# Optimization experiments

Measured on AMD Instinct MI355X. Metric: run time of the kernel, lower is better.

## Reference

```python
import jax, jax.numpy as jnp
import numpy as np

NA, NQ, FDIM, NC, HID = 512, 4096, 2, 16, 64
CUTOFF = 6.0
GAMMA = 10.0
BOX = 12.0


def setup_inputs() -> dict:
    key = jax.random.key(0)
    ks = jax.random.split(key, 16)
    s = lambda k, shp, fan: jax.random.normal(k, shp, jnp.float32) * (1.0 / np.sqrt(fan))
    return {
        "atom_pos": jax.random.uniform(ks[0], (NA, 3), jnp.float32) * BOX,
        "atom_feat": jax.random.normal(ks[1], (NA, FDIM), jnp.float32),
        "query_pos": jax.random.uniform(ks[2], (NQ, 3), jnp.float32) * BOX,
        "W1": s(ks[3], (FDIM + NC, HID), FDIM + NC), "b1": jnp.zeros((HID,), jnp.float32),
        "W2": s(ks[4], (HID, HID), HID), "b2": jnp.zeros((HID,), jnp.float32),
        "W3": s(ks[5], (HID, HID // 2), HID), "b3": jnp.zeros((HID // 2,), jnp.float32),
        "W4": s(ks[6], (HID // 2, 1), HID // 2), "b4": jnp.zeros((1,), jnp.float32),
        "W5": s(ks[7], (3, 64), 3), "b5": jnp.zeros((64,), jnp.float32),
        "W6": s(ks[8], (64, 3), 64), "b6": jnp.zeros((3,), jnp.float32),
    }


def _forward(atom_pos, atom_feat, query_pos, W1, b1, W2, b2, W3, b3, W4, b4, W5, b5, W6, b6):
    centers = jnp.linspace(0.0, CUTOFF, NC, dtype=jnp.float32)  # RBF centers
    rel = query_pos[:, None, :] - atom_pos[None, :, :]          # (Nq,Na,3)
    dist = jnp.linalg.norm(rel + 1e-12, axis=-1)                 # (Nq,Na) (matches torch.norm(rel+eps))
    mask = (dist <= CUTOFF).astype(dist.dtype)
    rbf = jnp.exp(-GAMMA * (dist[..., None] - centers) ** 2)     # (Nq,Na,Nc)
    feat_b = jnp.broadcast_to(atom_feat[None], (query_pos.shape[0],) + atom_feat.shape)
    atom_input = jnp.concatenate([feat_b, rbf], axis=-1)         # (Nq,Na,F+Nc)
    h = jax.nn.relu(atom_input @ W1 + b1)
    h = jax.nn.relu(h @ W2 + b2)                                 # (Nq,Na,H)
    scalar_w = (jax.nn.relu(h @ W3 + b3) @ W4 + b4)[..., 0] * mask  # (Nq,Na)
    dir_vec = rel / (dist[..., None] + 1e-12)                    # (Nq,Na,3)
    weighted = jnp.einsum('qa,qad->qd', scalar_w, dir_vec)       # (Nq,3)
    out = jax.nn.relu(weighted @ W5 + b5) @ W6 + b6              # (Nq,3)
    return out


def reference(atom_pos, atom_feat, query_pos, W1, b1, W2, b2, W3, b3, W4, b4, W5, b5, W6, b6):
    return _forward(atom_pos, atom_feat, query_pos, W1, b1, W2, b2, W3, b3, W4, b4, W5, b5, W6, b6)
```

## Files before the change

### kernel.cpp

```cpp
#include <hip/hip_runtime.h>
#include <math.h>


typedef _Float16 f16x4 __attribute__((ext_vector_type(4)));
typedef _Float16 f16x2 __attribute__((ext_vector_type(2)));
typedef float    f32x4 __attribute__((ext_vector_type(4)));

#define CAP 352
#define NT  2

__global__ __launch_bounds__(64) void repack_kernel(
    const float* __restrict__ W1, const float* __restrict__ b1,
    const float* __restrict__ W2, const float* __restrict__ b2,
    const float* __restrict__ W3, const float* __restrict__ b3,
    const float* __restrict__ W4, char* __restrict__ ws)
{
    const int b = blockIdx.x, l = threadIdx.x;
    const int col = l & 15, quad = l >> 4;
    if (b < 32) {
        f16x4 v;
        #pragma unroll
        for (int j = 0; j < 4; ++j) {
            float x;
            if (b < 8) {
                const int kc = b >> 2, mt = b & 3;
                const int k = kc*16 + quad*4 + j;
                x = (k < 18) ? W1[k*64 + mt*16 + col]
                             : (k == 18 ? b1[mt*16 + col] : 0.0f);
            } else if (b < 24) {
                const int idx = b - 8, kc = idx >> 2, mt = idx & 3;
                const int k = kc*16 + quad*4 + j;
                x = W2[k*64 + mt*16 + col];
            } else {
                const int idx = b - 24, kc = idx >> 1, mt = idx & 1;
                const int k = kc*16 + quad*4 + j;
                x = W3[k*32 + mt*16 + col];
            }
            v[j] = (_Float16)x;
        }
        *(f16x4*)(ws + (b*64 + l)*8) = v;
    } else {
        const int d = b - 32;
        float o[4];
        #pragma unroll
        for (int rr = 0; rr < 4; ++rr) {
            const int idx = quad*4 + rr;
            if (d < 4)      o[rr] = b2[d*16 + idx];
            else if (d < 6) o[rr] = b3[(d-4)*16 + idx];
            else            o[rr] = W4[(d-6)*16 + idx];
        }
        *(float4*)(ws + 16384 + (d*64 + l)*16) = make_float4(o[0],o[1],o[2],o[3]);
    }
}

__device__ __forceinline__ f16x4 relu_cvt(f32x4 c) {
    return f16x4{(_Float16)fmaxf(c[0],0.f), (_Float16)fmaxf(c[1],0.f),
                 (_Float16)fmaxf(c[2],0.f), (_Float16)fmaxf(c[3],0.f)};
}

__global__ __launch_bounds__(256, 1) void aqfn_kernel(
    const float* __restrict__ atom_pos,
    const float* __restrict__ atom_feat,
    const float* __restrict__ query_pos,
    const float* __restrict__ b4,
    const float* __restrict__ W5, const float* __restrict__ b5,
    const float* __restrict__ W6, const float* __restrict__ b6,
    const char*  __restrict__ ws,
    float* __restrict__ out)
{
    __shared__ __align__(16) float4 rbuf[CAP];
    __shared__ __align__(16) f16x2  fbuf[CAP];
    __shared__ float wred[4][3];
    __shared__ int   wcnt[4];

    const int tid  = threadIdx.x;
    const int wave = __builtin_amdgcn_readfirstlane(tid >> 6);
    const int lane = tid & 63;
    const int col  = lane & 15;
    const int quad = lane >> 4;
    const int q    = blockIdx.x;

    const f16x4*  wsf = (const f16x4*)ws;
    const float4* wsb = (const float4*)(ws + 16384);
    f16x4 w1f[2][4], w2f[4][4], w3f[4][2];
    #pragma unroll
    for (int kc = 0; kc < 2; ++kc)
        #pragma unroll
        for (int mt = 0; mt < 4; ++mt) w1f[kc][mt] = wsf[(kc*4 + mt)*64 + lane];
    #pragma unroll
    for (int kc = 0; kc < 4; ++kc)
        #pragma unroll
        for (int mt = 0; mt < 4; ++mt) w2f[kc][mt] = wsf[(8 + kc*4 + mt)*64 + lane];
    #pragma unroll
    for (int kc = 0; kc < 4; ++kc)
        #pragma unroll
        for (int mt = 0; mt < 2; ++mt) w3f[kc][mt] = wsf[(24 + kc*2 + mt)*64 + lane];
    float4 b2v[4], b3v[2], w4v[2];
    #pragma unroll
    for (int mt = 0; mt < 4; ++mt) b2v[mt] = wsb[mt*64 + lane];
    #pragma unroll
    for (int mt = 0; mt < 2; ++mt) { b3v[mt] = wsb[(4+mt)*64 + lane];
                                     w4v[mt] = wsb[(6+mt)*64 + lane]; }
    const float b4v = b4[0];

    const float qx = query_pos[q*3+0];
    const float qy = query_pos[q*3+1];
    const float qz = query_pos[q*3+2];

    float rxv[2], ryv[2], rzv[2], dv[2], f0v[2], f1v[2];
    unsigned long long msk[2];
    int mycnt = 0;
    #pragma unroll
    for (int it = 0; it < 2; ++it) {
        const int a = wave*128 + it*64 + lane;
        const float rx = qx - atom_pos[a*3+0];
        const float ry = qy - atom_pos[a*3+1];
        const float rz = qz - atom_pos[a*3+2];
        const float ex = __fadd_rn(rx, 1e-12f);
        const float ey = __fadd_rn(ry, 1e-12f);
        const float ez = __fadd_rn(rz, 1e-12f);
        const float dd = __fadd_rn(__fadd_rn(__fmul_rn(ex,ex), __fmul_rn(ey,ey)),
                                   __fmul_rn(ez,ez));
        const float dist = sqrtf(dd);
        rxv[it] = rx; ryv[it] = ry; rzv[it] = rz; dv[it] = dist;
        f0v[it] = atom_feat[a*2+0]; f1v[it] = atom_feat[a*2+1];
        msk[it] = __ballot(dist <= 6.0f);
        mycnt  += (int)__popcll(msk[it]);
    }
    if (lane == 0) wcnt[wave] = mycnt;
    __syncthreads();

    int base = 0, count = 0;
    #pragma unroll
    for (int w = 0; w < 4; ++w) {
        const int c = wcnt[w];
        if (w < wave) base += c;
        count += c;
    }
    if (count > CAP) count = CAP;

    {
        int off0 = base;
        #pragma unroll
        for (int it = 0; it < 2; ++it) {
            const bool in = (msk[it] >> lane) & 1ull;
            const int  p  = off0 + (int)__popcll(msk[it] & ((1ull << lane) - 1ull));
            if (in && p < CAP) {
                rbuf[p] = make_float4(rxv[it], ryv[it], rzv[it], dv[it]);
                fbuf[p] = f16x2{(_Float16)f0v[it], (_Float16)f1v[it]};
            }
            off0 += (int)__popcll(msk[it]);
        }
    }
    __syncthreads();

    float wacc0 = 0.f, wacc1 = 0.f, wacc2 = 0.f;
    const int nchunks = (count + (NT*16 - 1)) / (NT*16);

    #pragma unroll 1
    for (int chunk = wave; chunk < nchunks; chunk += 4) {
        const int row0 = chunk * (NT*16);

        float4 rv[NT]; f16x2 ffv[NT];
        #pragma unroll
        for (int u = 0; u < NT; ++u) {
            int pr = row0 + u*16 + col;
            if (pr >= count) pr = count - 1;
            rv[u]  = rbuf[pr];
            ffv[u] = fbuf[pr];
        }

        f16x4 xa[NT][2];
        #pragma unroll
        for (int u = 0; u < NT; ++u) {
            const float dist = rv[u].w;
            #pragma unroll
            for (int kc = 0; kc < 2; ++kc)
                #pragma unroll
                for (int j = 0; j < 4; ++j) {
                    const int k = kc*16 + quad*4 + j;
                    const float tt = dist - 0.4f * (float)(k - 2);
                    float v = __expf(-10.0f * tt * tt);
                    v = (k < 18) ? v : 0.0f;
                    _Float16 xv = (_Float16)v;
                    if (k == 18) xv = (_Float16)1.0f;
                    if (k == 0)  xv = ffv[u][0];
                    if (k == 1)  xv = ffv[u][1];
                    xa[u][kc][j] = xv;
                }
        }

        f16x4 a2[NT][4];
        #pragma unroll
        for (int u = 0; u < NT; ++u)
            #pragma unroll
            for (int mt = 0; mt < 4; ++mt) {
                f32x4 c = {0.f, 0.f, 0.f, 0.f};
                c = __builtin_amdgcn_mfma_f32_16x16x16f16(w1f[0][mt], xa[u][0], c, 0, 0, 0);
                c = __builtin_amdgcn_mfma_f32_16x16x16f16(w1f[1][mt], xa[u][1], c, 0, 0, 0);
                a2[u][mt] = relu_cvt(c);
            }

        f16x4 a3[NT][4];
        #pragma unroll
        for (int u = 0; u < NT; ++u)
            #pragma unroll
            for (int mt = 0; mt < 4; ++mt) {
                f32x4 c = {b2v[mt].x, b2v[mt].y, b2v[mt].z, b2v[mt].w};
                #pragma unroll
                for (int kc = 0; kc < 4; ++kc)
                    c = __builtin_amdgcn_mfma_f32_16x16x16f16(w2f[kc][mt], a2[u][kc], c, 0, 0, 0);
                a3[u][mt] = relu_cvt(c);
            }

        #pragma unroll
        for (int u = 0; u < NT; ++u) {
            float s = 0.f;
            #pragma unroll
            for (int mt = 0; mt < 2; ++mt) {
                f32x4 c = {b3v[mt].x, b3v[mt].y, b3v[mt].z, b3v[mt].w};
                #pragma unroll
                for (int kc = 0; kc < 4; ++kc)
                    c = __builtin_amdgcn_mfma_f32_16x16x16f16(w3f[kc][mt], a3[u][kc], c, 0, 0, 0);
                const float* wv = &w4v[mt].x;
                #pragma unroll
                for (int rr = 0; rr < 4; ++rr)
                    s = fmaf(fmaxf(c[rr], 0.f), wv[rr], s);
            }
            s += __shfl_xor(s, 16);
            s += __shfl_xor(s, 32);
            s += b4v;
            const int  p2  = row0 + u*16 + col;
            const bool vld = (p2 < count);
            const float inv = __builtin_amdgcn_rcpf(rv[u].w + 1e-12f);
            const float wm  = vld ? (s * inv) : 0.f;
            wacc0 = fmaf(wm, rv[u].x, wacc0);
            wacc1 = fmaf(wm, rv[u].y, wacc1);
            wacc2 = fmaf(wm, rv[u].z, wacc2);
        }
    }

    #pragma unroll
    for (int off = 1; off < 64; off <<= 1) {
        wacc0 += __shfl_xor(wacc0, off);
        wacc1 += __shfl_xor(wacc1, off);
        wacc2 += __shfl_xor(wacc2, off);
    }
    if (lane == 0) {
        wred[wave][0] = wacc0 * 0.25f;
        wred[wave][1] = wacc1 * 0.25f;
        wred[wave][2] = wacc2 * 0.25f;
    }
    __syncthreads();

    if (wave == 0) {
        const float v0 = wred[0][0] + wred[1][0] + wred[2][0] + wred[3][0];
        const float v1 = wred[0][1] + wred[1][1] + wred[2][1] + wred[3][1];
        const float v2 = wred[0][2] + wred[1][2] + wred[2][2] + wred[3][2];
        float th = fmaf(v0, W5[lane],
                   fmaf(v1, W5[64+lane],
                   fmaf(v2, W5[128+lane], b5[lane])));
        th = fmaxf(th, 0.f);
        float o0 = th * W6[lane*3+0];
        float o1 = th * W6[lane*3+1];
        float o2 = th * W6[lane*3+2];
        #pragma unroll
        for (int off = 1; off < 64; off <<= 1) {
            o0 += __shfl_xor(o0, off);
            o1 += __shfl_xor(o1, off);
            o2 += __shfl_xor(o2, off);
        }
        if (lane == 0) {
            out[q*3+0] = o0 + b6[0];
            out[q*3+1] = o1 + b6[1];
            out[q*3+2] = o2 + b6[2];
        }
    }
}

extern "C" void kernel_launch(void* const* d_in, const int* in_sizes, int n_in,
                              void* d_out, int out_size, void* d_ws, size_t ws_size,
                              hipStream_t stream) {
    const float* atom_pos  = (const float*)d_in[0];
    const float* atom_feat = (const float*)d_in[1];
    const float* query_pos = (const float*)d_in[2];
    const float* W1 = (const float*)d_in[3];  const float* b1 = (const float*)d_in[4];
    const float* W2 = (const float*)d_in[5];  const float* b2 = (const float*)d_in[6];
    const float* W3 = (const float*)d_in[7];  const float* b3 = (const float*)d_in[8];
    const float* W4 = (const float*)d_in[9];  const float* b4 = (const float*)d_in[10];
    const float* W5 = (const float*)d_in[11]; const float* b5 = (const float*)d_in[12];
    const float* W6 = (const float*)d_in[13]; const float* b6 = (const float*)d_in[14];
    float* out = (float*)d_out;
    char*  ws  = (char*)d_ws;

    hipLaunchKernelGGL(repack_kernel, dim3(40), dim3(64), 0, stream,
                       W1, b1, W2, b2, W3, b3, W4, ws);
    hipLaunchKernelGGL(aqfn_kernel, dim3(4096), dim3(256), 0, stream,
                       atom_pos, atom_feat, query_pos, b4, W5, b5, W6, b6,
                       (const char*)ws, out);
}
```

Measured before the change: 117.3 us.

## Process four queries per block with shared chunk scheduling across waves

Each 256-thread block now handles four queries, one wave compacting the in-cutoff atoms for each query. All four waves then pull 32-row chunks from a pooled list spanning every query in the block. This spreads the per-block weight-fragment loads over four queries and evens out uneven neighbour counts across waves. The cost is four times the LDS buffers, an extra sync barrier gone, twelve accumulators per lane with a branchy select, and a serial eight-step compaction loop per wave.

Result: slower. 125.1 us (+6.7%).

```diff
diff --git a/kernel.cpp b/kernel.cpp
--- a/kernel.cpp
+++ b/kernel.cpp
@@ -8,6 +8,7 @@
 
 #define CAP 352
 #define NT  2
+#define QPB 4
 
 __global__ __launch_bounds__(64) void repack_kernel(
     const float* __restrict__ W1, const float* __restrict__ b1,
@@ -68,17 +69,16 @@
     const char*  __restrict__ ws,
     float* __restrict__ out)
 {
-    __shared__ __align__(16) float4 rbuf[CAP];
-    __shared__ __align__(16) f16x2  fbuf[CAP];
-    __shared__ float wred[4][3];
-    __shared__ int   wcnt[4];
+    __shared__ __align__(16) float4 rbuf[QPB][CAP];
+    __shared__ __align__(16) f16x2  fbuf[QPB][CAP];
+    __shared__ float wred[4][QPB][3];
+    __shared__ int   cnt[QPB];
 
     const int tid  = threadIdx.x;
     const int wave = __builtin_amdgcn_readfirstlane(tid >> 6);
     const int lane = tid & 63;
     const int col  = lane & 15;
     const int quad = lane >> 4;
-    const int q    = blockIdx.x;
 
     const f16x4*  wsf = (const f16x4*)ws;
     const float4* wsb = (const float4*)(ws + 16384);
@@ -103,71 +103,70 @@
                                      w4v[mt] = wsb[(6+mt)*64 + lane]; }
     const float b4v = b4[0];
 
-    const float qx = query_pos[q*3+0];
-    const float qy = query_pos[q*3+1];
-    const float qz = query_pos[q*3+2];
-
-    float rxv[2], ryv[2], rzv[2], dv[2], f0v[2], f1v[2];
-    unsigned long long msk[2];
-    int mycnt = 0;
-    #pragma unroll
-    for (int it = 0; it < 2; ++it) {
-        const int a = wave*128 + it*64 + lane;
-        const float rx = qx - atom_pos[a*3+0];
-        const float ry = qy - atom_pos[a*3+1];
-        const float rz = qz - atom_pos[a*3+2];
-        const float ex = __fadd_rn(rx, 1e-12f);
-        const float ey = __fadd_rn(ry, 1e-12f);
-        const float ez = __fadd_rn(rz, 1e-12f);
-        const float dd = __fadd_rn(__fadd_rn(__fmul_rn(ex,ex), __fmul_rn(ey,ey)),
-                                   __fmul_rn(ez,ez));
-        const float dist = sqrtf(dd);
-        rxv[it] = rx; ryv[it] = ry; rzv[it] = rz; dv[it] = dist;
-        f0v[it] = atom_feat[a*2+0]; f1v[it] = atom_feat[a*2+1];
-        msk[it] = __ballot(dist <= 6.0f);
-        mycnt  += (int)__popcll(msk[it]);
-    }
-    if (lane == 0) wcnt[wave] = mycnt;
+    {
+        const int qg = blockIdx.x*QPB + wave;
+        const float qx = query_pos[qg*3+0];
+        const float qy = query_pos[qg*3+1];
+        const float qz = query_pos[qg*3+2];
+        int c = 0;
+        #pragma unroll 1
+        for (int it = 0; it < 8; ++it) {
+            const int a = it*64 + lane;
+            const float rx = qx - atom_pos[a*3+0];
+            const float ry = qy - atom_pos[a*3+1];
+            const float rz = qz - atom_pos[a*3+2];
+            const float ex = __fadd_rn(rx, 1e-12f);
+            const float ey = __fadd_rn(ry, 1e-12f);
+            const float ez = __fadd_rn(rz, 1e-12f);
+            const float dd = __fadd_rn(__fadd_rn(__fmul_rn(ex,ex), __fmul_rn(ey,ey)),
+                                       __fmul_rn(ez,ez));
+            const float dist = sqrtf(dd);
+            const bool  in   = (dist <= 6.0f);
+            const unsigned long long m = __ballot(in);
+            const int p = c + (int)__popcll(m & ((1ull << lane) - 1ull));
+            if (in && p < CAP) {
+                rbuf[wave][p] = make_float4(rx, ry, rz, dist);
+                fbuf[wave][p] = f16x2{(_Float16)atom_feat[a*2+0],
+                                      (_Float16)atom_feat[a*2+1]};
+            }
+            c += (int)__popcll(m);
+        }
+        if (c > CAP) c = CAP;
+        if (lane == 0) cnt[wave] = c;
+    }
     __syncthreads();
 
-    int base = 0, count = 0;
-    #pragma unroll
-    for (int w = 0; w < 4; ++w) {
-        const int c = wcnt[w];
-        if (w < wave) base += c;
-        count += c;
-    }
-    if (count > CAP) count = CAP;
-
-    {
-        int off0 = base;
-        #pragma unroll
-        for (int it = 0; it < 2; ++it) {
-            const bool in = (msk[it] >> lane) & 1ull;
-            const int  p  = off0 + (int)__popcll(msk[it] & ((1ull << lane) - 1ull));
-            if (in && p < CAP) {
-                rbuf[p] = make_float4(rxv[it], ryv[it], rzv[it], dv[it]);
-                fbuf[p] = f16x2{(_Float16)f0v[it], (_Float16)f1v[it]};
-            }
-            off0 += (int)__popcll(msk[it]);
-        }
-    }
-    __syncthreads();
-
-    float wacc0 = 0.f, wacc1 = 0.f, wacc2 = 0.f;
-    const int nchunks = (count + (NT*16 - 1)) / (NT*16);
+    int cntv[QPB], nch[QPB], cum[QPB];
+    int ntot = 0;
+    #pragma unroll
+    for (int w = 0; w < QPB; ++w) {
+        cntv[w] = cnt[w];
+        nch[w]  = (cntv[w] + (NT*16 - 1)) / (NT*16);
+        cum[w]  = ntot;
+        ntot   += nch[w];
+    }
+
+    float acc[QPB][3] = {{0,0,0},{0,0,0},{0,0,0},{0,0,0}};
 
     #pragma unroll 1
-    for (int chunk = wave; chunk < nchunks; chunk += 4) {
-        const int row0 = chunk * (NT*16);
+    for (int g = wave; g < ntot; g += 4) {
+        int cq = QPB - 1;
+        #pragma unroll
+        for (int w = QPB - 2; w >= 0; --w)
+            if (g < cum[w+1]) cq = w;
+        const int lc    = g - cum[cq];
+        const int count = cntv[cq];
+        const float4* __restrict__ rb = &rbuf[cq][0];
+        const f16x2*  __restrict__ fb = &fbuf[cq][0];
+        const int row0 = lc * (NT*16);
 
         float4 rv[NT]; f16x2 ffv[NT];
         #pragma unroll
         for (int u = 0; u < NT; ++u) {
             int pr = row0 + u*16 + col;
             if (pr >= count) pr = count - 1;
-            rv[u]  = rbuf[pr];
-            ffv[u] = fbuf[pr];
+            rv[u]  = rb[pr];
+            ffv[u] = fb[pr];
         }
 
         f16x4 xa[NT][2];
@@ -234,29 +233,37 @@
             const bool vld = (p2 < count);
             const float inv = __builtin_amdgcn_rcpf(rv[u].w + 1e-12f);
             const float wm  = vld ? (s * inv) : 0.f;
-            wacc0 = fmaf(wm, rv[u].x, wacc0);
-            wacc1 = fmaf(wm, rv[u].y, wacc1);
-            wacc2 = fmaf(wm, rv[u].z, wacc2);
-        }
-    }
-
-    #pragma unroll
-    for (int off = 1; off < 64; off <<= 1) {
-        wacc0 += __shfl_xor(wacc0, off);
-        wacc1 += __shfl_xor(wacc1, off);
-        wacc2 += __shfl_xor(wacc2, off);
-    }
-    if (lane == 0) {
-        wred[wave][0] = wacc0 * 0.25f;
-        wred[wave][1] = wacc1 * 0.25f;
-        wred[wave][2] = wacc2 * 0.25f;
-    }
+            if      (cq == 0) { acc[0][0] = fmaf(wm, rv[u].x, acc[0][0]);
+                                acc[0][1] = fmaf(wm, rv[u].y, acc[0][1]);
+                                acc[0][2] = fmaf(wm, rv[u].z, acc[0][2]); }
+            else if (cq == 1) { acc[1][0] = fmaf(wm, rv[u].x, acc[1][0]);
+                                acc[1][1] = fmaf(wm, rv[u].y, acc[1][1]);
+                                acc[1][2] = fmaf(wm, rv[u].z, acc[1][2]); }
+            else if (cq == 2) { acc[2][0] = fmaf(wm, rv[u].x, acc[2][0]);
+                                acc[2][1] = fmaf(wm, rv[u].y, acc[2][1]);
+                                acc[2][2] = fmaf(wm, rv[u].z, acc[2][2]); }
+            else              { acc[3][0] = fmaf(wm, rv[u].x, acc[3][0]);
+                                acc[3][1] = fmaf(wm, rv[u].y, acc[3][1]);
+                                acc[3][2] = fmaf(wm, rv[u].z, acc[3][2]); }
+        }
+    }
+
+    #pragma unroll
+    for (int w = 0; w < QPB; ++w)
+        #pragma unroll
+        for (int d = 0; d < 3; ++d) {
+            float v = acc[w][d];
+            #pragma unroll
+            for (int off = 1; off < 64; off <<= 1) v += __shfl_xor(v, off);
+            if (lane == 0) wred[wave][w][d] = v * 0.25f;
+        }
     __syncthreads();
 
-    if (wave == 0) {
-        const float v0 = wred[0][0] + wred[1][0] + wred[2][0] + wred[3][0];
-        const float v1 = wred[0][1] + wred[1][1] + wred[2][1] + wred[3][1];
-        const float v2 = wred[0][2] + wred[1][2] + wred[2][2] + wred[3][2];
+    {
+        const int w = wave;
+        const float v0 = wred[0][w][0] + wred[1][w][0] + wred[2][w][0] + wred[3][w][0];
+        const float v1 = wred[0][w][1] + wred[1][w][1] + wred[2][w][1] + wred[3][w][1];
+        const float v2 = wred[0][w][2] + wred[1][w][2] + wred[2][w][2] + wred[3][w][2];
         float th = fmaf(v0, W5[lane],
                    fmaf(v1, W5[64+lane],
                    fmaf(v2, W5[128+lane], b5[lane])));
@@ -271,9 +278,10 @@
             o2 += __shfl_xor(o2, off);
         }
         if (lane == 0) {
-            out[q*3+0] = o0 + b6[0];
-            out[q*3+1] = o1 + b6[1];
-            out[q*3+2] = o2 + b6[2];
+            const int qo = blockIdx.x*QPB + w;
+            out[qo*3+0] = o0 + b6[0];
+            out[qo*3+1] = o1 + b6[1];
+            out[qo*3+2] = o2 + b6[2];
         }
     }
 }
@@ -295,7 +303,7 @@
 
     hipLaunchKernelGGL(repack_kernel, dim3(40), dim3(64), 0, stream,
                        W1, b1, W2, b2, W3, b3, W4, ws);
-    hipLaunchKernelGGL(aqfn_kernel, dim3(4096), dim3(256), 0, stream,
+    hipLaunchKernelGGL(aqfn_kernel, dim3(4096 / QPB), dim3(256), 0, stream,
                        atom_pos, atom_feat, query_pos, b4, W5, b5, W6, b6,
                        (const char*)ws, out);
 }
```
